# Kernel optimization log

Measured on AMD Instinct MI355X. Metric: run time of the kernel, lower is better.

Reference implementation:

```python
import jax, jax.numpy as jnp
import numpy as np

BATCH = 4096
INPUT_SIZE = 8192
IO = 16            # inputoutput_dim
D_STATE = 32       # statespace_dim
N_STAGES = INPUT_SIZE // IO  # 512


def _glorot(key, shape):
    # glorot-uniform over the trailing matrix dims, matching get_random_glorot_uniform_matrix
    lim = float(np.sqrt(6.0 / (shape[-2] + shape[-1])))
    return jax.random.uniform(key, shape, minval=-lim, maxval=lim, dtype=jnp.float32)


def setup_inputs() -> dict:
    key = jax.random.key(0)
    ks = jax.random.split(key, 10)
    U = jax.random.normal(ks[0], (BATCH, INPUT_SIZE), dtype=jnp.float32)
    A = _glorot(ks[1], (N_STAGES, D_STATE, D_STATE))
    B = _glorot(ks[2], (N_STAGES, D_STATE, IO))
    C = _glorot(ks[3], (N_STAGES, IO, D_STATE))
    D = _glorot(ks[4], (N_STAGES, IO, IO))
    E = _glorot(ks[5], (N_STAGES, D_STATE, D_STATE))
    F = _glorot(ks[6], (N_STAGES, D_STATE, IO))
    G = _glorot(ks[7], (N_STAGES, IO, D_STATE))
    lim_b = float(np.sqrt(6.0 / INPUT_SIZE))
    bias = jax.random.uniform(ks[8], (INPUT_SIZE,), minval=-lim_b, maxval=lim_b, dtype=jnp.float32)
    return {"U": U, "A": A, "B": B, "C": C, "D": D, "E": E, "F": F, "G": G, "bias": bias}


def reference(U, A, B, C, D, E, F, G, bias):
    bt, p = U.shape
    n, io, d = C.shape
    u = U.reshape(bt, n, io).transpose(1, 0, 2)  # (N, batch, io)
    x0 = jnp.zeros((bt, d), dtype=U.dtype)

    # causal: y_k = C_k x_k + D_k u_k ; x_{k+1} = A_k x_k + B_k u_k, x_0 = 0
    def causal_step(x, inp):
        A_k, B_k, C_k, D_k, u_k = inp
        y_k = x @ C_k.T + u_k @ D_k.T
        x = x @ A_k.T + u_k @ B_k.T
        return x, y_k

    _, y_c = jax.lax.scan(causal_step, x0, (A, B, C, D, u))

    # anticausal (runs from last stage to first): y_k += G_k z_k ; z_{k-1} = E_k z_k + F_k u_k, z_N = 0
    def anti_step(z, inp):
        E_k, F_k, G_k, u_k = inp
        y_k = z @ G_k.T
        z = z @ E_k.T + u_k @ F_k.T
        return z, y_k

    _, y_a = jax.lax.scan(anti_step, x0, (E, F, G, u), reverse=True)

    y = (y_c + y_a).transpose(1, 0, 2).reshape(bt, p) + bias
    return y
```

## Files before the change

kernel.cpp:

```cpp
#include <hip/hip_runtime.h>


#define BATCH 4096
#define NCH   16
#define CHS   32
#define SROWS (BATCH + 32)
#define TSTR  36

typedef __attribute__((ext_vector_type(8))) short short8;
typedef __attribute__((ext_vector_type(4))) float f32x4;
typedef short8 __attribute__((may_alias)) short8a;
typedef f32x4 __attribute__((may_alias)) f32x4a;
typedef unsigned __attribute__((may_alias)) uinta;

#define MFMA16(a, b, c) __builtin_amdgcn_mfma_f32_16x16x32_bf16(a, b, c, 0, 0, 0)

__device__ __forceinline__ unsigned short bf16u(float x) {
  unsigned u = __builtin_bit_cast(unsigned, x);
  u += 0x7fffu + ((u >> 16) & 1u);
  return (unsigned short)(u >> 16);
}
__device__ __forceinline__ float bf2f(unsigned short u) {
  return __builtin_bit_cast(float, ((unsigned)u) << 16);
}
__device__ __forceinline__ unsigned pk2(float a, float b) {
  return (unsigned)bf16u(a) | (((unsigned)bf16u(b)) << 16);
}
template <int DT>
__device__ __forceinline__ const void* eptr(const void* b, long e) {
  return (const char*)b + e * (DT ? 4 : 2);
}

__device__ __forceinline__ void gload16(const void* g, void* lds) {
  __builtin_amdgcn_global_load_lds((const __attribute__((address_space(1))) void*)g,
                                   (__attribute__((address_space(3))) void*)lds, 16, 0, 0);
}
__device__ __forceinline__ void stage_blob8(const short* g, short* lds, int w, int lane) {
#pragma unroll
  for (int c = 0; c < 2; ++c) {
    const int ob = (w * 2 + c) * 1024;
    gload16((const char*)g + ob + lane * 16, (char*)lds + ob);
  }
}
__device__ __forceinline__ void stage_blob2k(const short* g, short* lds, int w, int lane) {
  if (w < 2) {
    const int ob = w * 1024;
    gload16((const char*)g + ob + lane * 16, (char*)lds + ob);
  }
}

template <int DT, int ROWS, int COLS, int PSTR>
__device__ __forceinline__ void stage2(const void* gp, short* hi, short* lo, int tid) {
  if constexpr (DT == 0) {
    const uinta* gu = (const uinta*)gp;
    for (int i = tid; i < ROWS * COLS / 2; i += 256) {
      int r = i / (COLS / 2), c = i - r * (COLS / 2);
      ((uinta*)(hi + r * PSTR))[c] = gu[i];
    }
  } else {
    const float* gf = (const float*)gp;
    for (int i = tid; i < ROWS * COLS; i += 256) {
      int r = i / COLS, c = i - r * COLS;
      float v = gf[i];
      unsigned short h = bf16u(v);
      hi[r * PSTR + c] = (short)h;
      lo[r * PSTR + c] = (short)bf16u(v - bf2f(h));
    }
  }
}
template <int DT, int ROWS, int COLS, int PSTR>
__device__ __forceinline__ void stage1(const void* gp, short* hi, int tid) {
  if constexpr (DT == 0) {
    const uinta* gu = (const uinta*)gp;
    for (int i = tid; i < ROWS * COLS / 2; i += 256) {
      int r = i / (COLS / 2), c = i - r * (COLS / 2);
      ((uinta*)(hi + r * PSTR))[c] = gu[i];
    }
  } else {
    const float* gf = (const float*)gp;
    for (int i = tid; i < ROWS * COLS; i += 256) {
      int r = i / COLS, c = i - r * COLS;
      hi[r * PSTR + c] = (short)bf16u(gf[i]);
    }
  }
}

__device__ __forceinline__ short8 ldfrag32(const short* l, int lane, int nbase) {
  int n = nbase + (lane & 15), q = lane >> 4;
  return *(const short8a*)(l + n * 40 + q * 8);
}
__device__ __forceinline__ short8 ldfrag16(const short* l, int lane, int nbase) {
  int n = nbase + (lane & 15), q = lane >> 4;
  short8 z = {};
  if (q < 2) z = *(const short8a*)(l + n * 24 + q * 8);
  return z;
}

__device__ __forceinline__ void twr(const f32x4* acc, float* T, int lane) {
  const int c = lane & 15, q = lane >> 4;
#pragma unroll
  for (int h = 0; h < 2; ++h)
#pragma unroll
    for (int r = 0; r < 4; ++r) T[(q * 4 + r) * TSTR + h * 16 + c] = acc[h][r];
}
__device__ __forceinline__ void trd(const float* T, int lane, short8& hi, short8& lo) {
  const int m = lane & 15, q = lane >> 4;
  const float* p = T + m * TSTR + q * 8;
#pragma unroll
  for (int j = 0; j < 8; ++j) {
    float v = p[j];
    unsigned short h = bf16u(v);
    hi[j] = (short)h;
    lo[j] = (short)bf16u(v - bf2f(h));
  }
}

template <int DT> struct URaw;
template <> struct URaw<0> { short8 s; };
template <> struct URaw<1> { f32x4 a, b; };

template <int DT>
__device__ __forceinline__ URaw<DT> ldu_raw(const void* U, size_t off) {
  URaw<DT> r;
  if constexpr (DT == 0) {
    r.s = *(const short8a*)((const short*)U + off);
  } else {
    const f32x4a* p = (const f32x4a*)((const float*)U + off);
    r.a = p[0];
    r.b = p[1];
  }
  return r;
}
template <int DT>
__device__ __forceinline__ void u_cvt(const URaw<DT>& r, short8& uhi, short8& ulo) {
  if constexpr (DT == 0) {
    uhi = r.s;
    ulo = short8{};
  } else {
#pragma unroll
    for (int j = 0; j < 4; ++j) {
      float v = r.a[j];
      unsigned short h = bf16u(v);
      uhi[j] = (short)h;
      ulo[j] = (short)bf16u(v - bf2f(h));
    }
#pragma unroll
    for (int j = 0; j < 4; ++j) {
      float v = r.b[j];
      unsigned short h = bf16u(v);
      uhi[4 + j] = (short)h;
      ulo[4 + j] = (short)bf16u(v - bf2f(h));
    }
  }
}
template <int DT, int MODE> struct UL {
  URaw<DT> r;
  __device__ __forceinline__ void fetch(const void* U, const short*, size_t row, int k, int qq) {
    r = ldu_raw<DT>(U, row * 8192 + (size_t)k * 16 + qq * 8);
  }
  __device__ __forceinline__ void get(short8& hi, short8& lo) const { u_cvt<DT>(r, hi, lo); }
};
template <> struct UL<1, 2> {
  short8 h, l;
  __device__ __forceinline__ void fetch(const void*, const short* Ub, size_t row, int k, int qq) {
    const short* p = Ub + (row * 1024 + (size_t)k * 2 + qq) * 16;
    h = *(const short8a*)p;
    l = *(const short8a*)(p + 8);
  }
  __device__ __forceinline__ void get(short8& hi, short8& lo) const { hi = h; lo = l; }
};

template <int DT>
__device__ __forceinline__ float ldbias(const void* b, int i) {
  if constexpr (DT == 0) return bf2f((unsigned short)((const short*)b)[i]);
  else return ((const float*)b)[i];
}

template <int DT>
__device__ __forceinline__ void step_state(const short8& Xhi, const short8& Xlo,
                                           const short8& uhi, const short8& ulo,
                                           const short* Mhi, const short* Mlo,
                                           const short* Bhi, const short* Blo,
                                           f32x4* out, int lane) {
#pragma unroll
  for (int h = 0; h < 2; ++h) {
    const f32x4 z4 = {0.f, 0.f, 0.f, 0.f};
    short8 bA = ldfrag32(Mhi, lane, h * 16);
    f32x4 ax = MFMA16(Xhi, bA, z4);
    ax = MFMA16(Xlo, bA, ax);
    short8 bB = ldfrag16(Bhi, lane, h * 16);
    ax = MFMA16(uhi, bB, ax);
    if constexpr (DT) {
      short8 bAl = ldfrag32(Mlo, lane, h * 16);
      ax = MFMA16(Xhi, bAl, ax);
      ax = MFMA16(ulo, bB, ax);
      short8 bBl = ldfrag16(Blo, lane, h * 16);
      ax = MFMA16(uhi, bBl, ax);
    }
    out[h] = ax;
  }
}

__global__ void k_detect(const unsigned short* __restrict__ U16, int* __restrict__ flag) {
  int lane = threadIdx.x;
  int bad = 0;
  for (int i = lane; i < 512; i += 64) {
    int e = (U16[i] >> 7) & 0xFF;
    bad += ((e > 134) || (e < 96 && e != 0)) ? 1 : 0;
  }
#pragma unroll
  for (int s = 32; s; s >>= 1) bad += __shfl_xor(bad, s);
  if (lane == 0) *flag = (bad > 48) ? 1 : 0;
}

template <int DT, int ROWS, int COLS, int PSTR, bool LO>
__device__ __forceinline__ void cvt_mat(const void* gp, short* hi, short* lo, int tid) {
  if constexpr (DT == 0) {
    const unsigned short* gs = (const unsigned short*)gp;
    for (int i = tid; i < ROWS * COLS; i += 256) {
      int r = i / COLS, c = i - r * COLS;
      hi[r * PSTR + c] = (short)gs[i];
    }
  } else {
    const float* gf = (const float*)gp;
    for (int i = tid; i < ROWS * COLS; i += 256) {
      int r = i / COLS, c = i - r * COLS;
      float v = gf[i];
      unsigned short h = bf16u(v);
      hi[r * PSTR + c] = (short)h;
      if constexpr (LO) lo[r * PSTR + c] = (short)bf16u(v - bf2f(h));
    }
  }
}
template <int DT>
__global__ __launch_bounds__(256) void k_prep(
    const int* __restrict__ flagp,
    const void* __restrict__ Am, const void* __restrict__ Bm, const void* __restrict__ Cm,
    const void* __restrict__ Dm, const void* __restrict__ Em, const void* __restrict__ Fm,
    const void* __restrict__ Gm,
    short* __restrict__ ABb, short* __restrict__ EFb, short* __restrict__ CDb,
    short* __restrict__ Gb) {
  if (*flagp != DT) return;
  const int k = blockIdx.x, tid = threadIdx.x;
  short* ab = ABb + (size_t)k * 4096;
  short* ef = EFb + (size_t)k * 4096;
  short* cd = CDb + (size_t)k * 1024;
  short* gb = Gb + (size_t)k * 1024;
  cvt_mat<DT, 32, 32, 40, true>(eptr<DT>(Am, (long)k * 1024), ab, ab + 1280, tid);
  cvt_mat<DT, 32, 16, 24, true>(eptr<DT>(Bm, (long)k * 512), ab + 2560, ab + 3328, tid);
  cvt_mat<DT, 32, 32, 40, true>(eptr<DT>(Em, (long)k * 1024), ef, ef + 1280, tid);
  cvt_mat<DT, 32, 16, 24, true>(eptr<DT>(Fm, (long)k * 512), ef + 2560, ef + 3328, tid);
  cvt_mat<DT, 16, 32, 40, false>(eptr<DT>(Cm, (long)k * 512), cd, nullptr, tid);
  cvt_mat<DT, 16, 16, 24, false>(eptr<DT>(Dm, (long)k * 256), cd + 640, nullptr, tid);
  cvt_mat<DT, 16, 32, 40, false>(eptr<DT>(Gm, (long)k * 512), gb, nullptr, tid);
}
__global__ __launch_bounds__(256) void k_prepU(const int* __restrict__ flagp,
                                               const float* __restrict__ Uf,
                                               short* __restrict__ Ub) {
  if (*flagp != 1) return;
  const size_t i = (size_t)blockIdx.x * 256 + threadIdx.x;
  const f32x4a* p = (const f32x4a*)(Uf + i * 8);
  f32x4 a = p[0], b = p[1];
  short8 hi, lo;
#pragma unroll
  for (int j = 0; j < 4; ++j) {
    unsigned short h = bf16u(a[j]);
    hi[j] = (short)h;
    lo[j] = (short)bf16u(a[j] - bf2f(h));
  }
#pragma unroll
  for (int j = 0; j < 4; ++j) {
    unsigned short h = bf16u(b[j]);
    hi[4 + j] = (short)h;
    lo[4 + j] = (short)bf16u(b[j] - bf2f(h));
  }
  *(short8a*)(Ub + i * 16) = hi;
  *(short8a*)(Ub + i * 16 + 8) = lo;
}

template <int DT, int MODE>
__global__ __launch_bounds__(256, 4) void k1_scan(
    const int* __restrict__ flagp, const void* __restrict__ U,
    const void* __restrict__ Am, const void* __restrict__ Bm,
    const void* __restrict__ Em, const void* __restrict__ Fm,
    const short* __restrict__ ABb, const short* __restrict__ EFb,
    const short* __restrict__ Ub,
    float* __restrict__ Sc, float* __restrict__ Sa) {
  if (*flagp != DT) return;
  const int ch = blockIdx.x, tile = blockIdx.y;
  const bool ident = (tile == 64);
  const int tid = threadIdx.x, lane = tid & 63, w = tid >> 6;
  const int s = ch * CHS;
  __shared__ __align__(16) short bAB[2][4096];
  __shared__ __align__(16) short bEF[2][4096];
  __shared__ __align__(16) float T[4][2][16 * TSTR];

  short8 Xhi = {}, Xlo = {}, Zhi = {}, Zlo = {};
  if (ident) {
    const int m = lane & 15, q = lane >> 4;
    short8 id = {};
#pragma unroll
    for (int j = 0; j < 8; ++j) id[j] = ((q * 8 + j) == (w * 16 + m)) ? (short)0x3F80 : (short)0;
    Xhi = id; Zhi = id;
  }

  auto stAB = [&](int k, int b) {
    if constexpr (MODE >= 1) {
      stage_blob8(ABb + (size_t)k * 4096, bAB[b], w, lane);
    } else {
      stage2<DT, 32, 32, 40>(eptr<DT>(Am, (long)k * 1024), bAB[b], bAB[b] + 1280, tid);
      stage2<DT, 32, 16, 24>(eptr<DT>(Bm, (long)k * 512), bAB[b] + 2560, bAB[b] + 3328, tid);
    }
  };
  auto stEF = [&](int k, int b) {
    if constexpr (MODE >= 1) {
      stage_blob8(EFb + (size_t)k * 4096, bEF[b], w, lane);
    } else {
      stage2<DT, 32, 32, 40>(eptr<DT>(Em, (long)k * 1024), bEF[b], bEF[b] + 1280, tid);
      stage2<DT, 32, 16, 24>(eptr<DT>(Fm, (long)k * 512), bEF[b] + 2560, bEF[b] + 3328, tid);
    }
  };

  stAB(s, 0);
  stEF(s + CHS - 1, 0);

  const size_t row = (size_t)(ident ? 0 : (tile * 64 + w * 16 + (lane & 15)));
  const int qq = (lane >> 4) & 1;
  UL<DT, MODE> upc, upa;
  if (!ident) {
    upc.fetch(U, Ub, row, s, qq);
    upa.fetch(U, Ub, row, s + CHS - 1, qq);
  }
  __syncthreads();

  f32x4 aX[2], aZ[2];
#pragma unroll 2
  for (int t = 0; t < CHS; ++t) {
    const int kc = s + t, ka = s + CHS - 1 - t, buf = t & 1;
    if (t < CHS - 1) {
      stAB(kc + 1, buf ^ 1);
      stEF(ka - 1, buf ^ 1);
    }
    short8 uch = {}, ucl = {}, uah = {}, ual = {};
    if (!ident) {
      upc.get(uch, ucl);
      upa.get(uah, ual);
      if (t < CHS - 1) {
        upc.fetch(U, Ub, row, kc + 1, qq);
        upa.fetch(U, Ub, row, ka - 1, qq);
      }
    }
    step_state<DT>(Xhi, Xlo, uch, ucl, bAB[buf], bAB[buf] + 1280, bAB[buf] + 2560,
                   bAB[buf] + 3328, aX, lane);
    step_state<DT>(Zhi, Zlo, uah, ual, bEF[buf], bEF[buf] + 1280, bEF[buf] + 2560,
                   bEF[buf] + 3328, aZ, lane);
    twr(aX, T[w][0], lane);
    twr(aZ, T[w][1], lane);
    trd(T[w][0], lane, Xhi, Xlo);
    trd(T[w][1], lane, Zhi, Zlo);
    __syncthreads();
  }

  if (!ident || w < 2) {
    const int grow = tile * 64 + w * 16;
#pragma unroll
    for (int h = 0; h < 2; ++h)
#pragma unroll
      for (int r = 0; r < 4; ++r) {
        const int m = (lane >> 4) * 4 + r, col = h * 16 + (lane & 15);
        const size_t off = ((size_t)ch * SROWS + grow + m) * 32 + col;
        Sc[off] = aX[h][r];
        Sa[off] = aZ[h][r];
      }
  }
}

__global__ __launch_bounds__(256) void k2_comb(float* __restrict__ Sc, float* __restrict__ Sa) {
  const int dir = blockIdx.y;
  const int r = threadIdx.x >> 5, j = threadIdx.x & 31;
  const int row = blockIdx.x * 8 + r;
  float* S = dir ? Sa : Sc;
  __shared__ float P[32][33];
  __shared__ float xs[8][33];
  float x = 0.f;
  for (int it = 0; it < NCH; ++it) {
    const int ch = dir ? (NCH - 1 - it) : it;
    const size_t base = ((size_t)ch * SROWS + row) * 32 + j;
    const float s_local = S[base];
    for (int i = threadIdx.x; i < 1024; i += 256)
      P[i >> 5][i & 31] = S[((size_t)ch * SROWS + BATCH + (i >> 5)) * 32 + (i & 31)];
    xs[r][j] = x;
    __syncthreads();
    S[base] = x;
    float acc = s_local;
#pragma unroll
    for (int m = 0; m < 32; ++m) acc += xs[r][m] * P[m][j];
    x = acc;
    __syncthreads();
  }
}

template <int DT, int MODE>
__global__ __launch_bounds__(256, 3) void k3_merged(
    const int* __restrict__ flagp, const void* __restrict__ U, const void* __restrict__ biasv,
    const short* __restrict__ ABb, const short* __restrict__ EFb,
    const short* __restrict__ CDb, const short* __restrict__ Gb,
    const short* __restrict__ Ub,
    const float* __restrict__ xin, const float* __restrict__ zin,
    void* __restrict__ out) {
  if (*flagp != DT) return;
  const int ch = blockIdx.x, tile = blockIdx.y;
  const int tid = threadIdx.x, lane = tid & 63, w = tid >> 6;
  const int s = ch * CHS;
  __shared__ __align__(16) short bAB[2][4096];
  __shared__ __align__(16) short bEF[2][4096];
  __shared__ __align__(16) short bCD[2][1024];
  __shared__ __align__(16) short bG[2][1024];
  __shared__ __align__(16) float T[4][16 * TSTR];

  const int cidx = lane & 15, quad = lane >> 4, qq = quad & 1;
  const size_t row = (size_t)(tile * 64 + w * 16 + cidx);

  short8 Xhi, Xlo, Zhi, Zlo;
  {
    const float* xp = xin + ((size_t)ch * SROWS + row) * 32 + quad * 8;
    const float* zp = zin + ((size_t)ch * SROWS + row) * 32 + quad * 8;
#pragma unroll
    for (int j = 0; j < 8; ++j) {
      float v = xp[j];
      unsigned short h = bf16u(v);
      Xhi[j] = (short)h;
      Xlo[j] = (short)bf16u(v - bf2f(h));
      float z = zp[j];
      unsigned short hz = bf16u(z);
      Zhi[j] = (short)hz;
      Zlo[j] = (short)bf16u(z - bf2f(hz));
    }
  }

  stage_blob8(ABb + (size_t)s * 4096, bAB[0], w, lane);
  stage_blob2k(CDb + (size_t)s * 1024, bCD[0], w, lane);
  stage_blob8(EFb + (size_t)(s + CHS - 1) * 4096, bEF[0], w, lane);
  stage_blob2k(Gb + (size_t)(s + CHS - 1) * 1024, bG[0], w, lane);
  UL<DT, MODE> upc, upa;
  upc.fetch(U, Ub, row, s, qq);
  upa.fetch(U, Ub, row, s + CHS - 1, qq);
  __syncthreads();

  f32x4 aX[2], aZ[2];
#pragma unroll 2
  for (int t = 0; t < CHS; ++t) {
    const int kc = s + t, ka = s + CHS - 1 - t, buf = t & 1;
    if (t < CHS - 1) {
      stage_blob8(ABb + (size_t)(kc + 1) * 4096, bAB[buf ^ 1], w, lane);
      stage_blob2k(CDb + (size_t)(kc + 1) * 1024, bCD[buf ^ 1], w, lane);
      stage_blob8(EFb + (size_t)(ka - 1) * 4096, bEF[buf ^ 1], w, lane);
      stage_blob2k(Gb + (size_t)(ka - 1) * 1024, bG[buf ^ 1], w, lane);
    }
    short8 uh, ul, vh, vl;
    upc.get(uh, ul);
    upa.get(vh, vl);
    if (t < CHS - 1) {
      upc.fetch(U, Ub, row, kc + 1, qq);
      upa.fetch(U, Ub, row, ka - 1, qq);
    }
    const f32x4 z4 = {0.f, 0.f, 0.f, 0.f};
    const short8 cf = ldfrag32(bCD[buf], lane, 0);
    f32x4 yc = MFMA16(Xhi, cf, z4);
    yc = MFMA16(Xlo, cf, yc);
    const short8 df = ldfrag16(bCD[buf] + 640, lane, 0);
    yc = MFMA16(uh, df, yc);
    if constexpr (DT) yc = MFMA16(ul, df, yc);
    const short8 gf = ldfrag32(bG[buf], lane, 0);
    f32x4 yz = MFMA16(Zhi, gf, z4);
    yz = MFMA16(Zlo, gf, yz);

    const float bv = ldbias<DT>(biasv, kc * 16 + cidx);
    const size_t rbase = (size_t)(tile * 64 + w * 16 + quad * 4) * 8192;
    const size_t oc = rbase + (size_t)kc * 16 + cidx;
    const size_t oa = rbase + (size_t)ka * 16 + cidx;
    if constexpr (DT == 0) {
      short* o = (short*)out;
      if (t < CHS / 2) {
#pragma unroll
        for (int r = 0; r < 4; ++r) o[oc + (size_t)r * 8192] = (short)bf16u(yc[r] + bv);
#pragma unroll
        for (int r = 0; r < 4; ++r) o[oa + (size_t)r * 8192] = (short)bf16u(yz[r]);
      } else {
#pragma unroll
        for (int r = 0; r < 4; ++r) {
          const float c = bf2f((unsigned short)o[oc + (size_t)r * 8192]);
          o[oc + (size_t)r * 8192] = (short)bf16u(c + yc[r] + bv);
        }
#pragma unroll
        for (int r = 0; r < 4; ++r) {
          const float c = bf2f((unsigned short)o[oa + (size_t)r * 8192]);
          o[oa + (size_t)r * 8192] = (short)bf16u(c + yz[r]);
        }
      }
    } else {
      float* o = (float*)out;
      if (t < CHS / 2) {
        *(uinta*)(o + oc) = pk2(yc[0] + bv, yc[1] + bv);
        *(uinta*)(o + oc + 2 * 8192) = pk2(yc[2] + bv, yc[3] + bv);
        *(uinta*)(o + oa) = pk2(yz[0], yz[1]);
        *(uinta*)(o + oa + 2 * 8192) = pk2(yz[2], yz[3]);
      } else {
        const unsigned p0 = *(const uinta*)(o + oc);
        const unsigned p1 = *(const uinta*)(o + oc + 2 * 8192);
        o[oc + 0 * 8192] = bf2f((unsigned short)(p0 & 0xffffu)) + yc[0] + bv;
        o[oc + 1 * 8192] = bf2f((unsigned short)(p0 >> 16)) + yc[1] + bv;
        o[oc + 2 * 8192] = bf2f((unsigned short)(p1 & 0xffffu)) + yc[2] + bv;
        o[oc + 3 * 8192] = bf2f((unsigned short)(p1 >> 16)) + yc[3] + bv;
        const unsigned q0 = *(const uinta*)(o + oa);
        const unsigned q1 = *(const uinta*)(o + oa + 2 * 8192);
        o[oa + 0 * 8192] = bf2f((unsigned short)(q0 & 0xffffu)) + yz[0];
        o[oa + 1 * 8192] = bf2f((unsigned short)(q0 >> 16)) + yz[1];
        o[oa + 2 * 8192] = bf2f((unsigned short)(q1 & 0xffffu)) + yz[2];
        o[oa + 3 * 8192] = bf2f((unsigned short)(q1 >> 16)) + yz[3];
      }
    }
    step_state<DT>(Xhi, Xlo, uh, ul, bAB[buf], bAB[buf] + 1280, bAB[buf] + 2560,
                   bAB[buf] + 3328, aX, lane);
    step_state<DT>(Zhi, Zlo, vh, vl, bEF[buf], bEF[buf] + 1280, bEF[buf] + 2560,
                   bEF[buf] + 3328, aZ, lane);
    twr(aX, T[w], lane);
    trd(T[w], lane, Xhi, Xlo);
    twr(aZ, T[w], lane);
    trd(T[w], lane, Zhi, Zlo);
    __syncthreads();
  }
}

template <int DT>
__global__ __launch_bounds__(256, 4) void k3_legacy(
    const int* __restrict__ flagp, const void* __restrict__ U,
    const void* __restrict__ Am, const void* __restrict__ Bm,
    const void* __restrict__ Cm, const void* __restrict__ Dm,
    const void* __restrict__ Em, const void* __restrict__ Fm,
    const void* __restrict__ Gm, const void* __restrict__ biasv,
    const float* __restrict__ xin, const float* __restrict__ zin,
    void* __restrict__ out) {
  if (*flagp != DT) return;
  const int ch = blockIdx.x, tile = blockIdx.y;
  const int tid = threadIdx.x, lane = tid & 63, w = tid >> 6;
  const int s = ch * CHS;
  __shared__ __align__(16) short bM[2][4096];
  __shared__ __align__(16) short bO[2][1024];
  __shared__ __align__(16) float T[4][16 * TSTR];
  const int cidx = lane & 15, quad = lane >> 4, qq = quad & 1;
  const size_t row = (size_t)(tile * 64 + w * 16 + cidx);

  auto stC = [&](int k, int b) {
    stage2<DT, 32, 32, 40>(eptr<DT>(Am, (long)k * 1024), bM[b], bM[b] + 1280, tid);
    stage2<DT, 32, 16, 24>(eptr<DT>(Bm, (long)k * 512), bM[b] + 2560, bM[b] + 3328, tid);
    stage1<DT, 16, 32, 40>(eptr<DT>(Cm, (long)k * 512), bO[b], tid);
    stage1<DT, 16, 16, 24>(eptr<DT>(Dm, (long)k * 256), bO[b] + 640, tid);
  };
  auto stA = [&](int k, int b) {
    stage2<DT, 32, 32, 40>(eptr<DT>(Em, (long)k * 1024), bM[b], bM[b] + 1280, tid);
    stage2<DT, 32, 16, 24>(eptr<DT>(Fm, (long)k * 512), bM[b] + 2560, bM[b] + 3328, tid);
    stage1<DT, 16, 32, 40>(eptr<DT>(Gm, (long)k * 512), bO[b], tid);
  };

  short8 Xhi, Xlo;
  {
    const float* xp = xin + ((size_t)ch * SROWS + row) * 32 + quad * 8;
#pragma unroll
    for (int j = 0; j < 8; ++j) {
      float v = xp[j];
      unsigned short h = bf16u(v);
      Xhi[j] = (short)h;
      Xlo[j] = (short)bf16u(v - bf2f(h));
    }
  }
  stC(s, 0);
  UL<DT, 0> up;
  up.fetch(U, nullptr, row, s, qq);
  __syncthreads();

  f32x4 aX[2];
#pragma unroll 2
  for (int t = 0; t < CHS; ++t) {
    const int k = s + t, buf = t & 1;
    if (t < CHS - 1) stC(k + 1, buf ^ 1);
    short8 uh, ul;
    up.get(uh, ul);
    if (t < CHS - 1) up.fetch(U, nullptr, row, k + 1, qq);
    const f32x4 z4 = {0.f, 0.f, 0.f, 0.f};
    const short8 cf = ldfrag32(bO[buf], lane, 0);
    f32x4 ya = MFMA16(Xhi, cf, z4);
    ya = MFMA16(Xlo, cf, ya);
    const short8 df = ldfrag16(bO[buf] + 640, lane, 0);
    ya = MFMA16(uh, df, ya);
    if constexpr (DT) ya = MFMA16(ul, df, ya);
    const float bv = ldbias<DT>(biasv, k * 16 + cidx);
    {
      const size_t obase = (size_t)(tile * 64 + w * 16 + quad * 4) * 8192 + (size_t)k * 16 + cidx;
      if constexpr (DT == 0) {
        short* o = (short*)out;
#pragma unroll
        for (int r = 0; r < 4; ++r) o[obase + (size_t)r * 8192] = (short)bf16u(ya[r] + bv);
      } else {
        float* o = (float*)out;
#pragma unroll
        for (int r = 0; r < 4; ++r) o[obase + (size_t)r * 8192] = ya[r] + bv;
      }
    }
    step_state<DT>(Xhi, Xlo, uh, ul, bM[buf], bM[buf] + 1280, bM[buf] + 2560, bM[buf] + 3328,
                   aX, lane);
    twr(aX, T[w], lane);
    trd(T[w], lane, Xhi, Xlo);
    __syncthreads();
  }

  short8 Zhi, Zlo;
  {
    const float* zp = zin + ((size_t)ch * SROWS + row) * 32 + quad * 8;
#pragma unroll
    for (int j = 0; j < 8; ++j) {
      float v = zp[j];
      unsigned short h = bf16u(v);
      Zhi[j] = (short)h;
      Zlo[j] = (short)bf16u(v - bf2f(h));
    }
  }
  stA(s + CHS - 1, 0);
  up.fetch(U, nullptr, row, s + CHS - 1, qq);
  __syncthreads();

  f32x4 aZ[2];
#pragma unroll 2
  for (int t = 0; t < CHS; ++t) {
    const int k = s + CHS - 1 - t, buf = t & 1;
    if (t < CHS - 1) stA(k - 1, buf ^ 1);
    short8 uh, ul;
    up.get(uh, ul);
    if (t < CHS - 1) up.fetch(U, nullptr, row, k - 1, qq);
    const f32x4 z4 = {0.f, 0.f, 0.f, 0.f};
    const short8 gf = ldfrag32(bO[buf], lane, 0);
    f32x4 ya = MFMA16(Zhi, gf, z4);
    ya = MFMA16(Zlo, gf, ya);
    {
      const size_t obase = (size_t)(tile * 64 + w * 16 + quad * 4) * 8192 + (size_t)k * 16 + cidx;
      if constexpr (DT == 0) {
        short* o = (short*)out;
#pragma unroll
        for (int r = 0; r < 4; ++r) {
          const float c = bf2f((unsigned short)o[obase + (size_t)r * 8192]);
          o[obase + (size_t)r * 8192] = (short)bf16u(c + ya[r]);
        }
      } else {
        float* o = (float*)out;
#pragma unroll
        for (int r = 0; r < 4; ++r) o[obase + (size_t)r * 8192] += ya[r];
      }
    }
    step_state<DT>(Zhi, Zlo, uh, ul, bM[buf], bM[buf] + 1280, bM[buf] + 2560, bM[buf] + 3328,
                   aZ, lane);
    twr(aZ, T[w], lane);
    trd(T[w], lane, Zhi, Zlo);
    __syncthreads();
  }
}

extern "C" void kernel_launch(void* const* d_in, const int* in_sizes, int n_in,
                              void* d_out, int out_size, void* d_ws, size_t ws_size,
                              hipStream_t stream) {
  (void)in_sizes; (void)n_in; (void)out_size;
  const void* U = d_in[0];
  const void* A = d_in[1];
  const void* B = d_in[2];
  const void* C = d_in[3];
  const void* D = d_in[4];
  const void* E = d_in[5];
  const void* F = d_in[6];
  const void* G = d_in[7];
  const void* bias = d_in[8];

  constexpr size_t SC1 = (size_t)NCH * SROWS * 32;
  constexpr size_t BLOBS = (size_t)512 * 8192 * 2 + (size_t)512 * 2048 * 2;
  constexpr size_t UBB = (size_t)BATCH * 1024 * 32;
  constexpr size_t NEED1 = 1024 + BLOBS + SC1 * 8;
  constexpr size_t NEED2 = NEED1 + UBB;
  const int mode = (ws_size >= NEED2) ? 2 : (ws_size >= NEED1 ? 1 : 0);

  char* base = (char*)d_ws;
  int* flag = (int*)base;
  short* ABb = (short*)(base + 1024);
  short* EFb = ABb + (size_t)512 * 4096;
  short* CDb = EFb + (size_t)512 * 4096;
  short* Gb = CDb + (size_t)512 * 1024;
  float* Sc = (mode >= 1) ? (float*)(Gb + (size_t)512 * 1024) : (float*)(base + 1024);
  float* Sa = Sc + SC1;
  short* Ub = (short*)(Sa + SC1);

  k_detect<<<1, 64, 0, stream>>>((const unsigned short*)U, flag);
  if (mode >= 1) {
    k_prep<0><<<512, 256, 0, stream>>>(flag, A, B, C, D, E, F, G, ABb, EFb, CDb, Gb);
    k_prep<1><<<512, 256, 0, stream>>>(flag, A, B, C, D, E, F, G, ABb, EFb, CDb, Gb);
  }
  if (mode == 2) k_prepU<<<16384, 256, 0, stream>>>(flag, (const float*)U, Ub);

  if (mode >= 1) {
    k1_scan<0, 1><<<dim3(NCH, 65), 256, 0, stream>>>(flag, U, A, B, E, F, ABb, EFb, Ub, Sc, Sa);
    if (mode == 2)
      k1_scan<1, 2><<<dim3(NCH, 65), 256, 0, stream>>>(flag, U, A, B, E, F, ABb, EFb, Ub, Sc, Sa);
    else
      k1_scan<1, 1><<<dim3(NCH, 65), 256, 0, stream>>>(flag, U, A, B, E, F, ABb, EFb, Ub, Sc, Sa);
    k2_comb<<<dim3(BATCH / 8, 2), 256, 0, stream>>>(Sc, Sa);
    k3_merged<0, 1><<<dim3(NCH, 64), 256, 0, stream>>>(flag, U, bias, ABb, EFb, CDb, Gb, Ub,
                                                       Sc, Sa, d_out);
    if (mode == 2)
      k3_merged<1, 2><<<dim3(NCH, 64), 256, 0, stream>>>(flag, U, bias, ABb, EFb, CDb, Gb, Ub,
                                                         Sc, Sa, d_out);
    else
      k3_merged<1, 1><<<dim3(NCH, 64), 256, 0, stream>>>(flag, U, bias, ABb, EFb, CDb, Gb, Ub,
                                                         Sc, Sa, d_out);
  } else {
    k1_scan<0, 0><<<dim3(NCH, 65), 256, 0, stream>>>(flag, U, A, B, E, F, ABb, EFb, Ub, Sc, Sa);
    k1_scan<1, 0><<<dim3(NCH, 65), 256, 0, stream>>>(flag, U, A, B, E, F, ABb, EFb, Ub, Sc, Sa);
    k2_comb<<<dim3(BATCH / 8, 2), 256, 0, stream>>>(Sc, Sa);
    k3_legacy<0><<<dim3(NCH, 64), 256, 0, stream>>>(flag, U, A, B, C, D, E, F, G, bias,
                                                    Sc, Sa, d_out);
    k3_legacy<1><<<dim3(NCH, 64), 256, 0, stream>>>(flag, U, A, B, C, D, E, F, G, bias,
                                                    Sc, Sa, d_out);
  }
}
```

Before: 605.4 us.

## Process two batch tiles per block in scan and output kernels

Each block of the chunk-scan and merged output kernels now handles two 64-row batch tiles, so the staged A/B/E/F and C/D/G fragments in LDS are reused by twice as many rows. The grids halve (65→33 and 64→32 in y), and the MFMA chains for both tiles are interleaved to give more independent work per wave. The aim is to cut LDS staging and fragment loads per row and to hide MFMA latency. In exchange, register pressure rises (launch bounds drop to 2 blocks per SM) and there are fewer blocks to spread across CUs.

```diff
diff --git a/kernel.cpp b/kernel.cpp
--- a/kernel.cpp
+++ b/kernel.cpp
@@ -198,6 +198,39 @@
       ax = MFMA16(uhi, bBl, ax);
     }
     out[h] = ax;
+  }
+}
+template <int DT>
+__device__ __forceinline__ void step_pair(const short8& X0h, const short8& X0l,
+                                          const short8& u0h, const short8& u0l,
+                                          const short8& X1h, const short8& X1l,
+                                          const short8& u1h, const short8& u1l,
+                                          const short* Mhi, const short* Mlo,
+                                          const short* Bhi, const short* Blo,
+                                          f32x4* o0, f32x4* o1, int lane) {
+#pragma unroll
+  for (int h = 0; h < 2; ++h) {
+    const f32x4 z4 = {0.f, 0.f, 0.f, 0.f};
+    short8 bA = ldfrag32(Mhi, lane, h * 16);
+    f32x4 a0 = MFMA16(X0h, bA, z4);
+    f32x4 a1 = MFMA16(X1h, bA, z4);
+    a0 = MFMA16(X0l, bA, a0);
+    a1 = MFMA16(X1l, bA, a1);
+    short8 bB = ldfrag16(Bhi, lane, h * 16);
+    a0 = MFMA16(u0h, bB, a0);
+    a1 = MFMA16(u1h, bB, a1);
+    if constexpr (DT) {
+      short8 bAl = ldfrag32(Mlo, lane, h * 16);
+      a0 = MFMA16(X0h, bAl, a0);
+      a1 = MFMA16(X1h, bAl, a1);
+      a0 = MFMA16(u0l, bB, a0);
+      a1 = MFMA16(u1l, bB, a1);
+      short8 bBl = ldfrag16(Blo, lane, h * 16);
+      a0 = MFMA16(u0h, bBl, a0);
+      a1 = MFMA16(u1h, bBl, a1);
+    }
+    o0[h] = a0;
+    o1[h] = a1;
   }
 }
 
@@ -279,12 +312,122 @@
 }
 
 template <int DT, int MODE>
-__global__ __launch_bounds__(256, 4) void k1_scan(
+__global__ __launch_bounds__(256, 2) void k1_dual(
+    const int* __restrict__ flagp, const void* __restrict__ U,
+    const short* __restrict__ ABb, const short* __restrict__ EFb,
+    const short* __restrict__ Ub,
+    float* __restrict__ Sc, float* __restrict__ Sa) {
+  if (*flagp != DT) return;
+  const int ch = blockIdx.x, y = blockIdx.y;
+  const int tile0 = (y < 32) ? 2 * y : 64, tile1 = (y < 32) ? 2 * y + 1 : 64;
+  const bool id0 = (tile0 == 64), id1 = (tile1 == 64);
+  const int tid = threadIdx.x, lane = tid & 63, w = tid >> 6;
+  const int s = ch * CHS;
+  __shared__ __align__(16) short bAB[2][4096];
+  __shared__ __align__(16) short bEF[2][4096];
+  __shared__ __align__(16) float T[4][16 * TSTR];
+
+  short8 X0h = {}, X0l = {}, Z0h = {}, Z0l = {};
+  short8 X1h = {}, X1l = {}, Z1h = {}, Z1l = {};
+  if (id0 || id1) {
+    const int m = lane & 15, q = lane >> 4;
+    short8 id = {};
+#pragma unroll
+    for (int j = 0; j < 8; ++j) id[j] = ((q * 8 + j) == (w * 16 + m)) ? (short)0x3F80 : (short)0;
+    if (id0) { X0h = id; Z0h = id; }
+    if (id1) { X1h = id; Z1h = id; }
+  }
+
+  stage_blob8(ABb + (size_t)s * 4096, bAB[0], w, lane);
+  stage_blob8(EFb + (size_t)(s + CHS - 1) * 4096, bEF[0], w, lane);
+
+  const size_t row0 = (size_t)(id0 ? 0 : (tile0 * 64 + w * 16 + (lane & 15)));
+  const size_t row1 = (size_t)(id1 ? 0 : (tile1 * 64 + w * 16 + (lane & 15)));
+  const int qq = (lane >> 4) & 1;
+  UL<DT, MODE> uc0, ua0, uc1, ua1;
+  if (!id0) {
+    uc0.fetch(U, Ub, row0, s, qq);
+    ua0.fetch(U, Ub, row0, s + CHS - 1, qq);
+  }
+  if (!id1) {
+    uc1.fetch(U, Ub, row1, s, qq);
+    ua1.fetch(U, Ub, row1, s + CHS - 1, qq);
+  }
+  __syncthreads();
+
+  f32x4 aX0[2], aZ0[2], aX1[2], aZ1[2];
+#pragma unroll 2
+  for (int t = 0; t < CHS; ++t) {
+    const int kc = s + t, ka = s + CHS - 1 - t, buf = t & 1;
+    if (t < CHS - 1) {
+      stage_blob8(ABb + (size_t)(kc + 1) * 4096, bAB[buf ^ 1], w, lane);
+      stage_blob8(EFb + (size_t)(ka - 1) * 4096, bEF[buf ^ 1], w, lane);
+    }
+    short8 c0h = {}, c0l = {}, a0h = {}, a0l = {};
+    short8 c1h = {}, c1l = {}, a1h = {}, a1l = {};
+    if (!id0) {
+      uc0.get(c0h, c0l);
+      ua0.get(a0h, a0l);
+      if (t < CHS - 1) {
+        uc0.fetch(U, Ub, row0, kc + 1, qq);
+        ua0.fetch(U, Ub, row0, ka - 1, qq);
+      }
+    }
+    if (!id1) {
+      uc1.get(c1h, c1l);
+      ua1.get(a1h, a1l);
+      if (t < CHS - 1) {
+        uc1.fetch(U, Ub, row1, kc + 1, qq);
+        ua1.fetch(U, Ub, row1, ka - 1, qq);
+      }
+    }
+    step_pair<DT>(X0h, X0l, c0h, c0l, X1h, X1l, c1h, c1l,
+                  bAB[buf], bAB[buf] + 1280, bAB[buf] + 2560, bAB[buf] + 3328, aX0, aX1, lane);
+    step_pair<DT>(Z0h, Z0l, a0h, a0l, Z1h, Z1l, a1h, a1l,
+                  bEF[buf], bEF[buf] + 1280, bEF[buf] + 2560, bEF[buf] + 3328, aZ0, aZ1, lane);
+    twr(aX0, T[w], lane);
+    trd(T[w], lane, X0h, X0l);
+    twr(aZ0, T[w], lane);
+    trd(T[w], lane, Z0h, Z0l);
+    twr(aX1, T[w], lane);
+    trd(T[w], lane, X1h, X1l);
+    twr(aZ1, T[w], lane);
+    trd(T[w], lane, Z1h, Z1l);
+    __syncthreads();
+  }
+
+  const int n = lane & 15, q = lane >> 4;
+  if (!id0 || w < 2) {
+    const int grow = tile0 * 64 + w * 16;
+#pragma unroll
+    for (int h = 0; h < 2; ++h)
+#pragma unroll
+      for (int r = 0; r < 4; ++r) {
+        const int m = q * 4 + r, col = h * 16 + n;
+        const size_t off = ((size_t)ch * SROWS + grow + m) * 32 + col;
+        Sc[off] = aX0[h][r];
+        Sa[off] = aZ0[h][r];
+      }
+  }
+  if (!id1 || w < 2) {
+    const int grow = tile1 * 64 + w * 16;
+#pragma unroll
+    for (int h = 0; h < 2; ++h)
+#pragma unroll
+      for (int r = 0; r < 4; ++r) {
+        const int m = q * 4 + r, col = h * 16 + n;
+        const size_t off = ((size_t)ch * SROWS + grow + m) * 32 + col;
+        Sc[off] = aX1[h][r];
+        Sa[off] = aZ1[h][r];
+      }
+  }
+}
+
+template <int DT>
+__global__ __launch_bounds__(256, 4) void k1_scan0(
     const int* __restrict__ flagp, const void* __restrict__ U,
     const void* __restrict__ Am, const void* __restrict__ Bm,
     const void* __restrict__ Em, const void* __restrict__ Fm,
-    const short* __restrict__ ABb, const short* __restrict__ EFb,
-    const short* __restrict__ Ub,
     float* __restrict__ Sc, float* __restrict__ Sa) {
   if (*flagp != DT) return;
   const int ch = blockIdx.x, tile = blockIdx.y;
@@ -293,7 +436,7 @@
   const int s = ch * CHS;
   __shared__ __align__(16) short bAB[2][4096];
   __shared__ __align__(16) short bEF[2][4096];
-  __shared__ __align__(16) float T[4][2][16 * TSTR];
+  __shared__ __align__(16) float T[4][16 * TSTR];
 
   short8 Xhi = {}, Xlo = {}, Zhi = {}, Zlo = {};
   if (ident) {
@@ -305,20 +448,12 @@
   }
 
   auto stAB = [&](int k, int b) {
-    if constexpr (MODE >= 1) {
-      stage_blob8(ABb + (size_t)k * 4096, bAB[b], w, lane);
-    } else {
-      stage2<DT, 32, 32, 40>(eptr<DT>(Am, (long)k * 1024), bAB[b], bAB[b] + 1280, tid);
-      stage2<DT, 32, 16, 24>(eptr<DT>(Bm, (long)k * 512), bAB[b] + 2560, bAB[b] + 3328, tid);
-    }
+    stage2<DT, 32, 32, 40>(eptr<DT>(Am, (long)k * 1024), bAB[b], bAB[b] + 1280, tid);
+    stage2<DT, 32, 16, 24>(eptr<DT>(Bm, (long)k * 512), bAB[b] + 2560, bAB[b] + 3328, tid);
   };
   auto stEF = [&](int k, int b) {
-    if constexpr (MODE >= 1) {
-      stage_blob8(EFb + (size_t)k * 4096, bEF[b], w, lane);
-    } else {
-      stage2<DT, 32, 32, 40>(eptr<DT>(Em, (long)k * 1024), bEF[b], bEF[b] + 1280, tid);
-      stage2<DT, 32, 16, 24>(eptr<DT>(Fm, (long)k * 512), bEF[b] + 2560, bEF[b] + 3328, tid);
-    }
+    stage2<DT, 32, 32, 40>(eptr<DT>(Em, (long)k * 1024), bEF[b], bEF[b] + 1280, tid);
+    stage2<DT, 32, 16, 24>(eptr<DT>(Fm, (long)k * 512), bEF[b] + 2560, bEF[b] + 3328, tid);
   };
 
   stAB(s, 0);
@@ -326,10 +461,10 @@
 
   const size_t row = (size_t)(ident ? 0 : (tile * 64 + w * 16 + (lane & 15)));
   const int qq = (lane >> 4) & 1;
-  UL<DT, MODE> upc, upa;
+  UL<DT, 0> upc, upa;
   if (!ident) {
-    upc.fetch(U, Ub, row, s, qq);
-    upa.fetch(U, Ub, row, s + CHS - 1, qq);
+    upc.fetch(U, nullptr, row, s, qq);
+    upa.fetch(U, nullptr, row, s + CHS - 1, qq);
   }
   __syncthreads();
 
@@ -346,18 +481,18 @@
       upc.get(uch, ucl);
       upa.get(uah, ual);
       if (t < CHS - 1) {
-        upc.fetch(U, Ub, row, kc + 1, qq);
-        upa.fetch(U, Ub, row, ka - 1, qq);
+        upc.fetch(U, nullptr, row, kc + 1, qq);
+        upa.fetch(U, nullptr, row, ka - 1, qq);
       }
     }
     step_state<DT>(Xhi, Xlo, uch, ucl, bAB[buf], bAB[buf] + 1280, bAB[buf] + 2560,
                    bAB[buf] + 3328, aX, lane);
     step_state<DT>(Zhi, Zlo, uah, ual, bEF[buf], bEF[buf] + 1280, bEF[buf] + 2560,
                    bEF[buf] + 3328, aZ, lane);
-    twr(aX, T[w][0], lane);
-    twr(aZ, T[w][1], lane);
-    trd(T[w][0], lane, Xhi, Xlo);
-    trd(T[w][1], lane, Zhi, Zlo);
+    twr(aX, T[w], lane);
+    trd(T[w], lane, Xhi, Xlo);
+    twr(aZ, T[w], lane);
+    trd(T[w], lane, Zhi, Zlo);
     __syncthreads();
   }
 
@@ -401,7 +536,7 @@
 }
 
 template <int DT, int MODE>
-__global__ __launch_bounds__(256, 3) void k3_merged(
+__global__ __launch_bounds__(256, 2) void k3_dual(
     const int* __restrict__ flagp, const void* __restrict__ U, const void* __restrict__ biasv,
     const short* __restrict__ ABb, const short* __restrict__ EFb,
     const short* __restrict__ CDb, const short* __restrict__ Gb,
@@ -409,7 +544,7 @@
     const float* __restrict__ xin, const float* __restrict__ zin,
     void* __restrict__ out) {
   if (*flagp != DT) return;
-  const int ch = blockIdx.x, tile = blockIdx.y;
+  const int ch = blockIdx.x, tile0 = blockIdx.y * 2, tile1 = tile0 + 1;
   const int tid = threadIdx.x, lane = tid & 63, w = tid >> 6;
   const int s = ch * CHS;
   __shared__ __align__(16) short bAB[2][4096];
@@ -419,35 +554,38 @@
   __shared__ __align__(16) float T[4][16 * TSTR];
 
   const int cidx = lane & 15, quad = lane >> 4, qq = quad & 1;
-  const size_t row = (size_t)(tile * 64 + w * 16 + cidx);
-
-  short8 Xhi, Xlo, Zhi, Zlo;
+  const size_t row0 = (size_t)(tile0 * 64 + w * 16 + cidx);
+  const size_t row1 = (size_t)(tile1 * 64 + w * 16 + cidx);
+
+  short8 X0h, X0l, Z0h, Z0l, X1h, X1l, Z1h, Z1l;
   {
-    const float* xp = xin + ((size_t)ch * SROWS + row) * 32 + quad * 8;
-    const float* zp = zin + ((size_t)ch * SROWS + row) * 32 + quad * 8;
-#pragma unroll
-    for (int j = 0; j < 8; ++j) {
-      float v = xp[j];
-      unsigned short h = bf16u(v);
-      Xhi[j] = (short)h;
-      Xlo[j] = (short)bf16u(v - bf2f(h));
-      float z = zp[j];
-      unsigned short hz = bf16u(z);
-      Zhi[j] = (short)hz;
-      Zlo[j] = (short)bf16u(z - bf2f(hz));
-    }
+    auto ld8 = [&](const float* p, short8& hi, short8& lo) {
+#pragma unroll
+      for (int j = 0; j < 8; ++j) {
+        float v = p[j];
+        unsigned short h = bf16u(v);
+        hi[j] = (short)h;
+        lo[j] = (short)bf16u(v - bf2f(h));
+      }
+    };
+    ld8(xin + ((size_t)ch * SROWS + row0) * 32 + quad * 8, X0h, X0l);
+    ld8(zin + ((size_t)ch * SROWS + row0) * 32 + quad * 8, Z0h, Z0l);
+    ld8(xin + ((size_t)ch * SROWS + row1) * 32 + quad * 8, X1h, X1l);
+    ld8(zin + ((size_t)ch * SROWS + row1) * 32 + quad * 8, Z1h, Z1l);
   }
 
   stage_blob8(ABb + (size_t)s * 4096, bAB[0], w, lane);
   stage_blob2k(CDb + (size_t)s * 1024, bCD[0], w, lane);
   stage_blob8(EFb + (size_t)(s + CHS - 1) * 4096, bEF[0], w, lane);
   stage_blob2k(Gb + (size_t)(s + CHS - 1) * 1024, bG[0], w, lane);
-  UL<DT, MODE> upc, upa;
-  upc.fetch(U, Ub, row, s, qq);
-  upa.fetch(U, Ub, row, s + CHS - 1, qq);
+  UL<DT, MODE> uc0, ua0, uc1, ua1;
+  uc0.fetch(U, Ub, row0, s, qq);
+  ua0.fetch(U, Ub, row0, s + CHS - 1, qq);
+  uc1.fetch(U, Ub, row1, s, qq);
+  ua1.fetch(U, Ub, row1, s + CHS - 1, qq);
   __syncthreads();
 
-  f32x4 aX[2], aZ[2];
+  f32x4 aX0[2], aZ0[2], aX1[2], aZ1[2];
 #pragma unroll 2
   for (int t = 0; t < CHS; ++t) {
     const int kc = s + t, ka = s + CHS - 1 - t, buf = t & 1;
@@ -457,77 +595,96 @@
       stage_blob8(EFb + (size_t)(ka - 1) * 4096, bEF[buf ^ 1], w, lane);
       stage_blob2k(Gb + (size_t)(ka - 1) * 1024, bG[buf ^ 1], w, lane);
     }
-    short8 uh, ul, vh, vl;
-    upc.get(uh, ul);
-    upa.get(vh, vl);
+    short8 u0h, u0l, v0h, v0l, u1h, u1l, v1h, v1l;
+    uc0.get(u0h, u0l);
+    ua0.get(v0h, v0l);
+    uc1.get(u1h, u1l);
+    ua1.get(v1h, v1l);
     if (t < CHS - 1) {
-      upc.fetch(U, Ub, row, kc + 1, qq);
-      upa.fetch(U, Ub, row, ka - 1, qq);
+      uc0.fetch(U, Ub, row0, kc + 1, qq);
+      ua0.fetch(U, Ub, row0, ka - 1, qq);
+      uc1.fetch(U, Ub, row1, kc + 1, qq);
+      ua1.fetch(U, Ub, row1, ka - 1, qq);
     }
     const f32x4 z4 = {0.f, 0.f, 0.f, 0.f};
     const short8 cf = ldfrag32(bCD[buf], lane, 0);
-    f32x4 yc = MFMA16(Xhi, cf, z4);
-    yc = MFMA16(Xlo, cf, yc);
     const short8 df = ldfrag16(bCD[buf] + 640, lane, 0);
-    yc = MFMA16(uh, df, yc);
-    if constexpr (DT) yc = MFMA16(ul, df, yc);
     const short8 gf = ldfrag32(bG[buf], lane, 0);
-    f32x4 yz = MFMA16(Zhi, gf, z4);
-    yz = MFMA16(Zlo, gf, yz);
+    f32x4 yc0 = MFMA16(X0h, cf, z4);
+    yc0 = MFMA16(X0l, cf, yc0);
+    yc0 = MFMA16(u0h, df, yc0);
+    if constexpr (DT) yc0 = MFMA16(u0l, df, yc0);
+    f32x4 yz0 = MFMA16(Z0h, gf, z4);
+    yz0 = MFMA16(Z0l, gf, yz0);
+    f32x4 yc1 = MFMA16(X1h, cf, z4);
+    yc1 = MFMA16(X1l, cf, yc1);
+    yc1 = MFMA16(u1h, df, yc1);
+    if constexpr (DT) yc1 = MFMA16(u1l, df, yc1);
+    f32x4 yz1 = MFMA16(Z1h, gf, z4);
+    yz1 = MFMA16(Z1l, gf, yz1);
 
     const float bv = ldbias<DT>(biasv, kc * 16 + cidx);
-    const size_t rbase = (size_t)(tile * 64 + w * 16 + quad * 4) * 8192;
-    const size_t oc = rbase + (size_t)kc * 16 + cidx;
-    const size_t oa = rbase + (size_t)ka * 16 + cidx;
-    if constexpr (DT == 0) {
-      short* o = (short*)out;
-      if (t < CHS / 2) {
-#pragma unroll
-        for (int r = 0; r < 4; ++r) o[oc + (size_t)r * 8192] = (short)bf16u(yc[r] + bv);
-#pragma unroll
-        for (int r = 0; r < 4; ++r) o[oa + (size_t)r * 8192] = (short)bf16u(yz[r]);
+    auto emit = [&](int tile, const f32x4& yc, const f32x4& yz) {
+      const size_t rbase = (size_t)(tile * 64 + w * 16 + quad * 4) * 8192;
+      const size_t oc = rbase + (size_t)kc * 16 + cidx;
+      const size_t oa = rbase + (size_t)ka * 16 + cidx;
+      if constexpr (DT == 0) {
+        short* o = (short*)out;
+        if (t < CHS / 2) {
+#pragma unroll
+          for (int r = 0; r < 4; ++r) o[oc + (size_t)r * 8192] = (short)bf16u(yc[r] + bv);
+#pragma unroll
+          for (int r = 0; r < 4; ++r) o[oa + (size_t)r * 8192] = (short)bf16u(yz[r]);
+        } else {
+#pragma unroll
+          for (int r = 0; r < 4; ++r) {
+            const float c = bf2f((unsigned short)o[oc + (size_t)r * 8192]);
+            o[oc + (size_t)r * 8192] = (short)bf16u(c + yc[r] + bv);
+          }
+#pragma unroll
+          for (int r = 0; r < 4; ++r) {
+            const float c = bf2f((unsigned short)o[oa + (size_t)r * 8192]);
+            o[oa + (size_t)r * 8192] = (short)bf16u(c + yz[r]);
+          }
+        }
       } else {
-#pragma unroll
-        for (int r = 0; r < 4; ++r) {
-          const float c = bf2f((unsigned short)o[oc + (size_t)r * 8192]);
-          o[oc + (size_t)r * 8192] = (short)bf16u(c + yc[r] + bv);
+        float* o = (float*)out;
+        if (t < CHS / 2) {
+          *(uinta*)(o + oc) = pk2(yc[0] + bv, yc[1] + bv);
+          *(uinta*)(o + oc + 2 * 8192) = pk2(yc[2] + bv, yc[3] + bv);
+          *(uinta*)(o + oa) = pk2(yz[0], yz[1]);
+          *(uinta*)(o + oa + 2 * 8192) = pk2(yz[2], yz[3]);
+        } else {
+          const unsigned p0 = *(const uinta*)(o + oc);
+          const unsigned p1 = *(const uinta*)(o + oc + 2 * 8192);
+          o[oc + 0 * 8192] = bf2f((unsigned short)(p0 & 0xffffu)) + yc[0] + bv;
+          o[oc + 1 * 8192] = bf2f((unsigned short)(p0 >> 16)) + yc[1] + bv;
+          o[oc + 2 * 8192] = bf2f((unsigned short)(p1 & 0xffffu)) + yc[2] + bv;
+          o[oc + 3 * 8192] = bf2f((unsigned short)(p1 >> 16)) + yc[3] + bv;
+          const unsigned q0 = *(const uinta*)(o + oa);
+          const unsigned q1 = *(const uinta*)(o + oa + 2 * 8192);
+          o[oa + 0 * 8192] = bf2f((unsigned short)(q0 & 0xffffu)) + yz[0];
+          o[oa + 1 * 8192] = bf2f((unsigned short)(q0 >> 16)) + yz[1];
+          o[oa + 2 * 8192] = bf2f((unsigned short)(q1 & 0xffffu)) + yz[2];
+          o[oa + 3 * 8192] = bf2f((unsigned short)(q1 >> 16)) + yz[3];
         }
-#pragma unroll
-        for (int r = 0; r < 4; ++r) {
-          const float c = bf2f((unsigned short)o[oa + (size_t)r * 8192]);
-          o[oa + (size_t)r * 8192] = (short)bf16u(c + yz[r]);
-        }
-      }
-    } else {
-      float* o = (float*)out;
-      if (t < CHS / 2) {
-        *(uinta*)(o + oc) = pk2(yc[0] + bv, yc[1] + bv);
-        *(uinta*)(o + oc + 2 * 8192) = pk2(yc[2] + bv, yc[3] + bv);
-        *(uinta*)(o + oa) = pk2(yz[0], yz[1]);
-        *(uinta*)(o + oa + 2 * 8192) = pk2(yz[2], yz[3]);
-      } else {
-        const unsigned p0 = *(const uinta*)(o + oc);
-        const unsigned p1 = *(const uinta*)(o + oc + 2 * 8192);
-        o[oc + 0 * 8192] = bf2f((unsigned short)(p0 & 0xffffu)) + yc[0] + bv;
-        o[oc + 1 * 8192] = bf2f((unsigned short)(p0 >> 16)) + yc[1] + bv;
-        o[oc + 2 * 8192] = bf2f((unsigned short)(p1 & 0xffffu)) + yc[2] + bv;
-        o[oc + 3 * 8192] = bf2f((unsigned short)(p1 >> 16)) + yc[3] + bv;
-        const unsigned q0 = *(const uinta*)(o + oa);
-        const unsigned q1 = *(const uinta*)(o + oa + 2 * 8192);
-        o[oa + 0 * 8192] = bf2f((unsigned short)(q0 & 0xffffu)) + yz[0];
-        o[oa + 1 * 8192] = bf2f((unsigned short)(q0 >> 16)) + yz[1];
-        o[oa + 2 * 8192] = bf2f((unsigned short)(q1 & 0xffffu)) + yz[2];
-        o[oa + 3 * 8192] = bf2f((unsigned short)(q1 >> 16)) + yz[3];
-      }
-    }
-    step_state<DT>(Xhi, Xlo, uh, ul, bAB[buf], bAB[buf] + 1280, bAB[buf] + 2560,
-                   bAB[buf] + 3328, aX, lane);
-    step_state<DT>(Zhi, Zlo, vh, vl, bEF[buf], bEF[buf] + 1280, bEF[buf] + 2560,
-                   bEF[buf] + 3328, aZ, lane);
-    twr(aX, T[w], lane);
-    trd(T[w], lane, Xhi, Xlo);
-    twr(aZ, T[w], lane);
-    trd(T[w], lane, Zhi, Zlo);
+      }
+    };
+    emit(tile0, yc0, yz0);
+    emit(tile1, yc1, yz1);
+
+    step_pair<DT>(X0h, X0l, u0h, u0l, X1h, X1l, u1h, u1l,
+                  bAB[buf], bAB[buf] + 1280, bAB[buf] + 2560, bAB[buf] + 3328, aX0, aX1, lane);
+    step_pair<DT>(Z0h, Z0l, v0h, v0l, Z1h, Z1l, v1h, v1l,
+                  bEF[buf], bEF[buf] + 1280, bEF[buf] + 2560, bEF[buf] + 3328, aZ0, aZ1, lane);
+    twr(aX0, T[w], lane);
+    trd(T[w], lane, X0h, X0l);
+    twr(aZ0, T[w], lane);
+    trd(T[w], lane, Z0h, Z0l);
+    twr(aX1, T[w], lane);
+    trd(T[w], lane, X1h, X1l);
+    twr(aZ1, T[w], lane);
+    trd(T[w], lane, Z1h, Z1l);
     __syncthreads();
   }
 }
@@ -703,23 +860,23 @@
   if (mode == 2) k_prepU<<<16384, 256, 0, stream>>>(flag, (const float*)U, Ub);
 
   if (mode >= 1) {
-    k1_scan<0, 1><<<dim3(NCH, 65), 256, 0, stream>>>(flag, U, A, B, E, F, ABb, EFb, Ub, Sc, Sa);
+    k1_dual<0, 1><<<dim3(NCH, 33), 256, 0, stream>>>(flag, U, ABb, EFb, Ub, Sc, Sa);
     if (mode == 2)
-      k1_scan<1, 2><<<dim3(NCH, 65), 256, 0, stream>>>(flag, U, A, B, E, F, ABb, EFb, Ub, Sc, Sa);
+      k1_dual<1, 2><<<dim3(NCH, 33), 256, 0, stream>>>(flag, U, ABb, EFb, Ub, Sc, Sa);
     else
-      k1_scan<1, 1><<<dim3(NCH, 65), 256, 0, stream>>>(flag, U, A, B, E, F, ABb, EFb, Ub, Sc, Sa);
+      k1_dual<1, 1><<<dim3(NCH, 33), 256, 0, stream>>>(flag, U, ABb, EFb, Ub, Sc, Sa);
     k2_comb<<<dim3(BATCH / 8, 2), 256, 0, stream>>>(Sc, Sa);
-    k3_merged<0, 1><<<dim3(NCH, 64), 256, 0, stream>>>(flag, U, bias, ABb, EFb, CDb, Gb, Ub,
+    k3_dual<0, 1><<<dim3(NCH, 32), 256, 0, stream>>>(flag, U, bias, ABb, EFb, CDb, Gb, Ub,
+                                                     Sc, Sa, d_out);
+    if (mode == 2)
+      k3_dual<1, 2><<<dim3(NCH, 32), 256, 0, stream>>>(flag, U, bias, ABb, EFb, CDb, Gb, Ub,
                                                        Sc, Sa, d_out);
-    if (mode == 2)
-      k3_merged<1, 2><<<dim3(NCH, 64), 256, 0, stream>>>(flag, U, bias, ABb, EFb, CDb, Gb, Ub,
-                                                         Sc, Sa, d_out);
     else
-      k3_merged<1, 1><<<dim3(NCH, 64), 256, 0, stream>>>(flag, U, bias, ABb, EFb, CDb, Gb, Ub,
-                                                         Sc, Sa, d_out);
+      k3_dual<1, 1><<<dim3(NCH, 32), 256, 0, stream>>>(flag, U, bias, ABb, EFb, CDb, Gb, Ub,
+                                                       Sc, Sa, d_out);
   } else {
-    k1_scan<0, 0><<<dim3(NCH, 65), 256, 0, stream>>>(flag, U, A, B, E, F, ABb, EFb, Ub, Sc, Sa);
-    k1_scan<1, 0><<<dim3(NCH, 65), 256, 0, stream>>>(flag, U, A, B, E, F, ABb, EFb, Ub, Sc, Sa);
+    k1_scan0<0><<<dim3(NCH, 65), 256, 0, stream>>>(flag, U, A, B, E, F, Sc, Sa);
+    k1_scan0<1><<<dim3(NCH, 65), 256, 0, stream>>>(flag, U, A, B, E, F, Sc, Sa);
     k2_comb<<<dim3(BATCH / 8, 2), 256, 0, stream>>>(Sc, Sa);
     k3_legacy<0><<<dim3(NCH, 64), 256, 0, stream>>>(flag, U, A, B, C, D, E, F, G, bias,
                                                     Sc, Sa, d_out);
```

Result: slower. 630.0 us (+4.1%).
